# Optimization experiments

Hardware: AMD Instinct MI355X
Metric: run time of the kernel (lower is better)

The kernel has to match this reference:

```python
import jax, jax.numpy as jnp
import numpy as np

N_NODES = 100000
N_EDGES = 1600000
D = 64
NUM_GROUPS = 2


def setup_inputs() -> dict:
    key = jax.random.key(0)
    k_h, k_ws, k_wg, k_src, k_dst, k_grp = jax.random.split(key, 6)
    h = jax.random.normal(k_h, (N_NODES, D), dtype=jnp.float32)
    # nn.Linear(in, out, bias=False) weights have shape [out, in]
    W_self = jax.random.normal(k_ws, (D, D), dtype=jnp.float32) * (1.0 / np.sqrt(D))
    W_groups = jax.random.normal(k_wg, (NUM_GROUPS, D, D), dtype=jnp.float32) * (1.0 / np.sqrt(D))
    src = jax.random.randint(k_src, (N_EDGES,), 0, N_NODES, dtype=jnp.int32)
    dst = jax.random.randint(k_dst, (N_EDGES,), 0, N_NODES, dtype=jnp.int32)
    group_labels = jax.random.randint(k_grp, (N_NODES,), 0, NUM_GROUPS, dtype=jnp.int32)
    return {"h": h, "W_self": W_self, "W_groups": W_groups,
            "src": src, "dst": dst, "group_labels": group_labels}


def reference(h, W_self, W_groups, src, dst, group_labels):
    # h: [N, d_in]; W_self: [d_out, d_in]; W_groups: [G, d_out, d_in]
    # Edge list (src, dst) replaces the DGL graph; message m_e = h[src_e],
    # transformed by W_groups[group[src_e]], scatter-added into dst_e.
    n_nodes = h.shape[0]
    num_groups = W_groups.shape[0]

    h_self = h @ W_self.T                       # [N, d_out]

    h_src = jnp.take(h, src, axis=0)            # [E, d_in] edge gather
    g_src = jnp.take(group_labels, src, axis=0)  # [E]

    h_agg = jnp.zeros((n_nodes, W_groups.shape[1]), dtype=h.dtype)
    for i in range(num_groups):  # small fixed loop over groups
        masked = jnp.where((g_src == i)[:, None], h_src, 0.0)  # [E, d_in]
        # Linearity lets us aggregate first, then transform (same math as
        # transforming each message then scatter_add, but far less compute).
        seg = jax.ops.segment_sum(masked, dst, num_segments=n_nodes)  # [N, d_in]
        h_agg = h_agg + seg @ W_groups[i].T      # [N, d_out]

    return h_self + h_agg
```

## Files before the change

kernel.cpp:

```cpp
#include <hip/hip_runtime.h>

#define N_NODES 100000
#define N_EDGES 1600000
#define D 64
#define NB2 3125
#define NR 2
#define CAPB_R 384
#define LCAP 64
#define LSTR 68
#define SRC_MASK 0x1FFFF
#define NBB 782
#define ZOFF (N_NODES * 32)

typedef unsigned int u32;
typedef short bfrag8 __attribute__((ext_vector_type(8)));
typedef float f32x4 __attribute__((ext_vector_type(4)));


__device__ inline u32 pk_bf16(float lo, float hi) {
    u32 a = __float_as_uint(lo);
    a = (a + 0x7fffu + ((a >> 16) & 1u)) >> 16;
    u32 b = __float_as_uint(hi);
    b = (b + 0x7fffu + ((b >> 16) & 1u)) & 0xffff0000u;
    return a | b;
}

__global__ __launch_bounds__(256) void prep(const float* __restrict__ h,
                                            const float* __restrict__ W_self,
                                            const float* __restrict__ W_groups,
                                            const int* __restrict__ src,
                                            const int* __restrict__ dst,
                                            const int* __restrict__ grp,
                                            int* __restrict__ bcnt,
                                            int* __restrict__ buckets,
                                            u32* __restrict__ h_bf,
                                            u32* __restrict__ Wc) {
    __shared__ int hist[NB2];
    __shared__ int gbase[NB2];
    const int tid = threadIdx.x;
    const int bx = blockIdx.x;

    if (bx < NBB) {
        const int r = bx & (NR - 1);
        for (int b = tid; b < NB2; b += 256) hist[b] = 0;
        __syncthreads();

        int ent[8], bkt[8], rnk[8];
        const int e0 = bx * 2048;
#pragma unroll
        for (int i = 0; i < 8; ++i) {
            int e = e0 + tid + i * 256;
            if (e < N_EDGES) {
                int s = src[e], d = dst[e];
                int g = grp[s];
                bkt[i] = d >> 5;
                ent[i] = s | (g << 17) | ((d & 31) << 18);
                rnk[i] = atomicAdd(&hist[bkt[i]], 1);
            } else {
                bkt[i] = -1;
            }
        }
        __syncthreads();
        for (int b = tid; b < NB2; b += 256) {
            int hc = hist[b];
            gbase[b] = hc ? atomicAdd(&bcnt[b * NR + r], hc) : 0;
        }
        __syncthreads();
#pragma unroll
        for (int i = 0; i < 8; ++i) {
            if (bkt[i] >= 0) {
                int pos = gbase[bkt[i]] + rnk[i];
                if (pos < CAPB_R)
                    buckets[(bkt[i] * NR + r) * CAPB_R + pos] = ent[i];
            }
        }
    } else if (bx < NBB + 12500) {
        int i = (bx - NBB) * 256 + tid;
        float2 v = reinterpret_cast<const float2*>(h)[i];
        h_bf[i] = pk_bf16(v.x, v.y);
    } else {
        for (int idx = tid; idx < 6144; idx += 256) {
            int j = idx / 96, kk = idx - j * 96;
            int k = kk * 2;
            float lo, hi;
            if (k < 64)       { lo = W_self[j * 64 + k];          hi = W_self[j * 64 + k + 1]; }
            else if (k < 128) { lo = W_groups[j * 64 + k - 64];   hi = W_groups[j * 64 + k - 63]; }
            else              { lo = W_groups[4096 + j * 64 + k - 128];
                                hi = W_groups[4096 + j * 64 + k - 127]; }
            Wc[j * 96 + kk] = pk_bf16(lo, hi);
        }
        if (tid < 32) h_bf[ZOFF + tid] = 0u;
    }
}

__global__ __launch_bounds__(256, 8) void gather_gemm(const u32* __restrict__ h_bf,
                                                      const int* __restrict__ bcnt,
                                                      const int* __restrict__ buckets,
                                                      const u32* __restrict__ Wc,
                                                      float* __restrict__ out) {
    __shared__ __align__(16) int lcsr[32 * LSTR];
    __shared__ int cntg[64];

    const int tid = threadIdx.x;
    const int cb = blockIdx.x;
    const int nbase = cb * 32;

    if (tid < 64) cntg[tid] = 0;
    __syncthreads();

    {
        const int2 cc = *reinterpret_cast<const int2*>(bcnt + cb * NR);
        int cns[NR] = { cc.x, cc.y };
#pragma unroll
        for (int r = 0; r < NR; ++r) {
            const int cnt = min(cns[r], CAPB_R);
            const int* bp = buckets + (cb * NR + r) * CAPB_R;
            for (int i = tid; i < cnt; i += 256) {
                int e = bp[i];
                int nl = (e >> 18) & 31;
                int g = (e >> 17) & 1;
                int off = (e & SRC_MASK) * 32;
                int idx = atomicAdd(&cntg[g * 32 + nl], 1);
                int pos = g ? (LCAP - 1 - idx) : idx;
                if (idx < LCAP) lcsr[nl * LSTR + pos] = off;
            }
        }
    }
    __syncthreads();

    const int wave = tid >> 6;
    const int lane = tid & 63;
    const int half = lane >> 5;
    const int c = lane & 31;

    for (int q = 0; q < 8; ++q) {
        const int nl = wave * 8 + q;
        const int base = nl * LSTR;
        const int c0 = min(cntg[nl], LCAP);
        const int c1 = min(cntg[32 + nl], LCAP);
        const int total = c0 + c1;
        float a0l = 0.f, a0h = 0.f, a1l = 0.f, a1h = 0.f;

        for (int i = 0; i < total; i += 8) {
            if (i + 8 <= c0) {
                int off[4];
#pragma unroll
                for (int k = 0; k < 4; ++k)
                    off[k] = lcsr[base + i + 2 * k + half];
                u32 x[4];
#pragma unroll
                for (int k = 0; k < 4; ++k) x[k] = h_bf[(size_t)(off[k] + c)];
#pragma unroll
                for (int k = 0; k < 4; ++k) {
                    a0l += __uint_as_float(x[k] << 16);
                    a0h += __uint_as_float(x[k] & 0xffff0000u);
                }
            } else if (i >= c0) {
                int off[4];
#pragma unroll
                for (int k = 0; k < 4; ++k) {
                    int u = i + 2 * k + half;
                    int idx = (LCAP - 1 - (u - c0)) & (LCAP - 1);
                    int v = lcsr[base + idx];
                    off[k] = (u < total) ? v : ZOFF;
                }
                u32 x[4];
#pragma unroll
                for (int k = 0; k < 4; ++k) x[k] = h_bf[(size_t)(off[k] + c)];
#pragma unroll
                for (int k = 0; k < 4; ++k) {
                    a1l += __uint_as_float(x[k] << 16);
                    a1h += __uint_as_float(x[k] & 0xffff0000u);
                }
            } else {
                int off[4];
                bool fm[4];
#pragma unroll
                for (int k = 0; k < 4; ++k) {
                    int u = i + 2 * k + half;
                    bool f = u < c0;
                    int idx = f ? u : ((LCAP - 1 - (u - c0)) & (LCAP - 1));
                    int v = lcsr[base + idx];
                    off[k] = (u < total) ? v : ZOFF;
                    fm[k] = f;
                }
                u32 x[4];
#pragma unroll
                for (int k = 0; k < 4; ++k) x[k] = h_bf[(size_t)(off[k] + c)];
#pragma unroll
                for (int k = 0; k < 4; ++k) {
                    float vl = __uint_as_float(x[k] << 16);
                    float vh = __uint_as_float(x[k] & 0xffff0000u);
                    a0l += fm[k] ? vl : 0.f;
                    a0h += fm[k] ? vh : 0.f;
                    a1l += fm[k] ? 0.f : vl;
                    a1h += fm[k] ? 0.f : vh;
                }
            }
        }

        a0l += __shfl_xor(a0l, 32, 64);
        a0h += __shfl_xor(a0h, 32, 64);
        a1l += __shfl_xor(a1l, 32, 64);
        a1h += __shfl_xor(a1h, 32, 64);

        if (half == 0) {
            lcsr[base + c]      = (int)pk_bf16(a0l, a0h);
            lcsr[base + 32 + c] = (int)pk_bf16(a1l, a1h);
        }
    }
    __syncthreads();

    const int m = lane & 15;
    const int quad = lane >> 4;
    const int rowh = wave & 1;
    const int jth = wave >> 1;
    const int nl16 = rowh * 16 + m;
    const int arow = nbase + nl16;

    union Cvt { uint4 u; bfrag8 s; };
    bfrag8 a[6];
    const u32* ap = h_bf + (size_t)arow * 32 + quad * 4;
#pragma unroll
    for (int ks = 0; ks < 2; ++ks) {
        Cvt cv;
        cv.u = *reinterpret_cast<const uint4*>(ap + ks * 16);
        a[ks] = cv.s;
    }
#pragma unroll
    for (int ks = 2; ks < 6; ++ks) {
        Cvt cv;
        cv.u = *reinterpret_cast<const uint4*>(&lcsr[nl16 * LSTR + (ks - 2) * 16 + quad * 4]);
        a[ks] = cv.s;
    }

    f32x4 acc[2];
#pragma unroll
    for (int jj = 0; jj < 2; ++jj) acc[jj] = (f32x4){0.f, 0.f, 0.f, 0.f};

    const u32* wp = Wc + (size_t)m * 96 + quad * 4;
#pragma unroll
    for (int ks = 0; ks < 6; ++ks) {
#pragma unroll
        for (int jj = 0; jj < 2; ++jj) {
            Cvt cw;
            cw.u = *reinterpret_cast<const uint4*>(wp + (jth * 2 + jj) * 1536 + ks * 16);
            acc[jj] = __builtin_amdgcn_mfma_f32_16x16x32_bf16(a[ks], cw.s, acc[jj], 0, 0, 0);
        }
    }

    const int rbase = nbase + rowh * 16 + quad * 4;
#pragma unroll
    for (int jj = 0; jj < 2; ++jj) {
#pragma unroll
        for (int r = 0; r < 4; ++r) {
            out[(size_t)(rbase + r) * 64 + (jth * 2 + jj) * 16 + m] = acc[jj][r];
        }
    }
}

extern "C" void kernel_launch(void* const* d_in, const int* in_sizes, int n_in,
                              void* d_out, int out_size, void* d_ws, size_t ws_size,
                              hipStream_t stream) {
    const float* h        = (const float*)d_in[0];
    const float* W_self   = (const float*)d_in[1];
    const float* W_groups = (const float*)d_in[2];
    const int*   src      = (const int*)d_in[3];
    const int*   dst      = (const int*)d_in[4];
    const int*   grp      = (const int*)d_in[5];
    float*       out      = (float*)d_out;

    int* bcnt    = (int*)d_ws;
    int* buckets = bcnt + 8192;
    u32* h_bf    = (u32*)(buckets + NB2 * NR * CAPB_R);
    u32* Wc      = h_bf + (size_t)N_NODES * 32 + 32;

    hipMemsetAsync(bcnt, 0, 8192 * sizeof(int), stream);

    prep<<<NBB + 12500 + 1, 256, 0, stream>>>(h, W_self, W_groups, src, dst, grp,
                                              bcnt, buckets, h_bf, Wc);
    gather_gemm<<<NB2, 256, 0, stream>>>(h_bf, bcnt, buckets, Wc, out);
}
```

Measured before the change: 192.3 us.

## Use direct global atomics for bucketing and split the gather loop by group

The prep kernel drops its shared-memory histogram and two-pass bucket placement and instead takes one global atomicAdd per edge, choosing the sub-bucket from the edge index parity. Each packed entry now stores a byte offset so the gather can use it directly. The gather loop is split into separate per-group loops that read four offsets with one vector LDS load and skip the mixed-group masking. The bf16 conversion handles four floats per thread. The aim is fewer barriers and fewer instructions in the bucketing and gather stages, at the cost of much heavier global atomic contention on the bucket counters.

```diff
diff --git a/kernel.cpp b/kernel.cpp
--- a/kernel.cpp
+++ b/kernel.cpp
@@ -8,9 +8,9 @@
 #define CAPB_R 384
 #define LCAP 64
 #define LSTR 68
-#define SRC_MASK 0x1FFFF
 #define NBB 782
-#define ZOFF (N_NODES * 32)
+#define NTC 6250
+#define ZB ((u32)(N_NODES * 128))
 
 typedef unsigned int u32;
 typedef short bfrag8 __attribute__((ext_vector_type(8)));
@@ -35,17 +35,10 @@
                                             int* __restrict__ buckets,
                                             u32* __restrict__ h_bf,
                                             u32* __restrict__ Wc) {
-    __shared__ int hist[NB2];
-    __shared__ int gbase[NB2];
     const int tid = threadIdx.x;
     const int bx = blockIdx.x;
 
     if (bx < NBB) {
-        const int r = bx & (NR - 1);
-        for (int b = tid; b < NB2; b += 256) hist[b] = 0;
-        __syncthreads();
-
-        int ent[8], bkt[8], rnk[8];
         const int e0 = bx * 2048;
 #pragma unroll
         for (int i = 0; i < 8; ++i) {
@@ -53,31 +46,17 @@
             if (e < N_EDGES) {
                 int s = src[e], d = dst[e];
                 int g = grp[s];
-                bkt[i] = d >> 5;
-                ent[i] = s | (g << 17) | ((d & 31) << 18);
-                rnk[i] = atomicAdd(&hist[bkt[i]], 1);
-            } else {
-                bkt[i] = -1;
+                int cidx = (d >> 5) * NR + (e & 1);
+                u32 ent = ((u32)s << 7) | ((u32)g << 5) | (u32)(d & 31);
+                int pos = atomicAdd(&bcnt[cidx], 1);
+                if (pos < CAPB_R) buckets[cidx * CAPB_R + pos] = (int)ent;
             }
         }
-        __syncthreads();
-        for (int b = tid; b < NB2; b += 256) {
-            int hc = hist[b];
-            gbase[b] = hc ? atomicAdd(&bcnt[b * NR + r], hc) : 0;
-        }
-        __syncthreads();
-#pragma unroll
-        for (int i = 0; i < 8; ++i) {
-            if (bkt[i] >= 0) {
-                int pos = gbase[bkt[i]] + rnk[i];
-                if (pos < CAPB_R)
-                    buckets[(bkt[i] * NR + r) * CAPB_R + pos] = ent[i];
-            }
-        }
-    } else if (bx < NBB + 12500) {
+    } else if (bx < NBB + NTC) {
         int i = (bx - NBB) * 256 + tid;
-        float2 v = reinterpret_cast<const float2*>(h)[i];
-        h_bf[i] = pk_bf16(v.x, v.y);
+        float4 v = reinterpret_cast<const float4*>(h)[i];
+        h_bf[2 * i]     = pk_bf16(v.x, v.y);
+        h_bf[2 * i + 1] = pk_bf16(v.z, v.w);
     } else {
         for (int idx = tid; idx < 6144; idx += 256) {
             int j = idx / 96, kk = idx - j * 96;
@@ -89,7 +68,7 @@
                                 hi = W_groups[4096 + j * 64 + k - 127]; }
             Wc[j * 96 + kk] = pk_bf16(lo, hi);
         }
-        if (tid < 32) h_bf[ZOFF + tid] = 0u;
+        if (tid < 32) h_bf[N_NODES * 32 + tid] = 0u;
     }
 }
 
@@ -116,13 +95,13 @@
             const int cnt = min(cns[r], CAPB_R);
             const int* bp = buckets + (cb * NR + r) * CAPB_R;
             for (int i = tid; i < cnt; i += 256) {
-                int e = bp[i];
-                int nl = (e >> 18) & 31;
-                int g = (e >> 17) & 1;
-                int off = (e & SRC_MASK) * 32;
+                u32 e = (u32)bp[i];
+                int nl = e & 31;
+                int g = (e >> 5) & 1;
+                u32 off = e & 0xFFFFFF80u;
                 int idx = atomicAdd(&cntg[g * 32 + nl], 1);
                 int pos = g ? (LCAP - 1 - idx) : idx;
-                if (idx < LCAP) lcsr[nl * LSTR + pos] = off;
+                if (idx < LCAP) lcsr[nl * LSTR + pos] = (int)off;
             }
         }
     }
@@ -131,72 +110,72 @@
     const int wave = tid >> 6;
     const int lane = tid & 63;
     const int half = lane >> 5;
-    const int c = lane & 31;
+    const u32 c4 = (u32)((lane & 31) * 4);
+    const char* hb = (const char*)h_bf;
 
     for (int q = 0; q < 8; ++q) {
         const int nl = wave * 8 + q;
         const int base = nl * LSTR;
         const int c0 = min(cntg[nl], LCAP);
         const int c1 = min(cntg[32 + nl], LCAP);
-        const int total = c0 + c1;
         float a0l = 0.f, a0h = 0.f, a1l = 0.f, a1h = 0.f;
 
-        for (int i = 0; i < total; i += 8) {
-            if (i + 8 <= c0) {
-                int off[4];
-#pragma unroll
-                for (int k = 0; k < 4; ++k)
-                    off[k] = lcsr[base + i + 2 * k + half];
-                u32 x[4];
-#pragma unroll
-                for (int k = 0; k < 4; ++k) x[k] = h_bf[(size_t)(off[k] + c)];
-#pragma unroll
-                for (int k = 0; k < 4; ++k) {
-                    a0l += __uint_as_float(x[k] << 16);
-                    a0h += __uint_as_float(x[k] & 0xffff0000u);
-                }
-            } else if (i >= c0) {
-                int off[4];
-#pragma unroll
-                for (int k = 0; k < 4; ++k) {
-                    int u = i + 2 * k + half;
-                    int idx = (LCAP - 1 - (u - c0)) & (LCAP - 1);
-                    int v = lcsr[base + idx];
-                    off[k] = (u < total) ? v : ZOFF;
-                }
-                u32 x[4];
-#pragma unroll
-                for (int k = 0; k < 4; ++k) x[k] = h_bf[(size_t)(off[k] + c)];
-#pragma unroll
-                for (int k = 0; k < 4; ++k) {
-                    a1l += __uint_as_float(x[k] << 16);
-                    a1h += __uint_as_float(x[k] & 0xffff0000u);
-                }
-            } else {
-                int off[4];
-                bool fm[4];
-#pragma unroll
-                for (int k = 0; k < 4; ++k) {
-                    int u = i + 2 * k + half;
-                    bool f = u < c0;
-                    int idx = f ? u : ((LCAP - 1 - (u - c0)) & (LCAP - 1));
-                    int v = lcsr[base + idx];
-                    off[k] = (u < total) ? v : ZOFF;
-                    fm[k] = f;
-                }
-                u32 x[4];
-#pragma unroll
-                for (int k = 0; k < 4; ++k) x[k] = h_bf[(size_t)(off[k] + c)];
-#pragma unroll
-                for (int k = 0; k < 4; ++k) {
-                    float vl = __uint_as_float(x[k] << 16);
-                    float vh = __uint_as_float(x[k] & 0xffff0000u);
-                    a0l += fm[k] ? vl : 0.f;
-                    a0h += fm[k] ? vh : 0.f;
-                    a1l += fm[k] ? 0.f : vl;
-                    a1h += fm[k] ? 0.f : vh;
-                }
-            }
+        int i = 0;
+        for (; i + 8 <= c0; i += 8) {
+            int4 w = *reinterpret_cast<const int4*>(&lcsr[base + i + 4 * half]);
+            u32 x0 = *(const u32*)(hb + ((u32)w.x + c4));
+            u32 x1 = *(const u32*)(hb + ((u32)w.y + c4));
+            u32 x2 = *(const u32*)(hb + ((u32)w.z + c4));
+            u32 x3 = *(const u32*)(hb + ((u32)w.w + c4));
+            a0l += __uint_as_float(x0 << 16); a0h += __uint_as_float(x0 & 0xffff0000u);
+            a0l += __uint_as_float(x1 << 16); a0h += __uint_as_float(x1 & 0xffff0000u);
+            a0l += __uint_as_float(x2 << 16); a0h += __uint_as_float(x2 & 0xffff0000u);
+            a0l += __uint_as_float(x3 << 16); a0h += __uint_as_float(x3 & 0xffff0000u);
+        }
+        if (i < c0) {
+            int4 w = *reinterpret_cast<const int4*>(&lcsr[base + i + 4 * half]);
+            int u = i + 4 * half;
+            u32 o0 = (u + 0 < c0) ? (u32)w.x : ZB;
+            u32 o1 = (u + 1 < c0) ? (u32)w.y : ZB;
+            u32 o2 = (u + 2 < c0) ? (u32)w.z : ZB;
+            u32 o3 = (u + 3 < c0) ? (u32)w.w : ZB;
+            u32 x0 = *(const u32*)(hb + (o0 + c4));
+            u32 x1 = *(const u32*)(hb + (o1 + c4));
+            u32 x2 = *(const u32*)(hb + (o2 + c4));
+            u32 x3 = *(const u32*)(hb + (o3 + c4));
+            a0l += __uint_as_float(x0 << 16); a0h += __uint_as_float(x0 & 0xffff0000u);
+            a0l += __uint_as_float(x1 << 16); a0h += __uint_as_float(x1 & 0xffff0000u);
+            a0l += __uint_as_float(x2 << 16); a0h += __uint_as_float(x2 & 0xffff0000u);
+            a0l += __uint_as_float(x3 << 16); a0h += __uint_as_float(x3 & 0xffff0000u);
+        }
+
+        int j = 0;
+        for (; j + 8 <= c1; j += 8) {
+            int4 w = *reinterpret_cast<const int4*>(&lcsr[base + (LCAP - 4) - j - 4 * half]);
+            u32 x0 = *(const u32*)(hb + ((u32)w.x + c4));
+            u32 x1 = *(const u32*)(hb + ((u32)w.y + c4));
+            u32 x2 = *(const u32*)(hb + ((u32)w.z + c4));
+            u32 x3 = *(const u32*)(hb + ((u32)w.w + c4));
+            a1l += __uint_as_float(x0 << 16); a1h += __uint_as_float(x0 & 0xffff0000u);
+            a1l += __uint_as_float(x1 << 16); a1h += __uint_as_float(x1 & 0xffff0000u);
+            a1l += __uint_as_float(x2 << 16); a1h += __uint_as_float(x2 & 0xffff0000u);
+            a1l += __uint_as_float(x3 << 16); a1h += __uint_as_float(x3 & 0xffff0000u);
+        }
+        if (j < c1) {
+            int4 w = *reinterpret_cast<const int4*>(&lcsr[base + (LCAP - 4) - j - 4 * half]);
+            int u = j + 4 * half;
+            u32 o0 = (u + 3 < c1) ? (u32)w.x : ZB;
+            u32 o1 = (u + 2 < c1) ? (u32)w.y : ZB;
+            u32 o2 = (u + 1 < c1) ? (u32)w.z : ZB;
+            u32 o3 = (u + 0 < c1) ? (u32)w.w : ZB;
+            u32 x0 = *(const u32*)(hb + (o0 + c4));
+            u32 x1 = *(const u32*)(hb + (o1 + c4));
+            u32 x2 = *(const u32*)(hb + (o2 + c4));
+            u32 x3 = *(const u32*)(hb + (o3 + c4));
+            a1l += __uint_as_float(x0 << 16); a1h += __uint_as_float(x0 & 0xffff0000u);
+            a1l += __uint_as_float(x1 << 16); a1h += __uint_as_float(x1 & 0xffff0000u);
+            a1l += __uint_as_float(x2 << 16); a1h += __uint_as_float(x2 & 0xffff0000u);
+            a1l += __uint_as_float(x3 << 16); a1h += __uint_as_float(x3 & 0xffff0000u);
         }
 
         a0l += __shfl_xor(a0l, 32, 64);
@@ -205,6 +184,7 @@
         a1h += __shfl_xor(a1h, 32, 64);
 
         if (half == 0) {
+            const int c = lane & 31;
             lcsr[base + c]      = (int)pk_bf16(a0l, a0h);
             lcsr[base + 32 + c] = (int)pk_bf16(a1l, a1h);
         }
@@ -277,7 +257,7 @@
 
     hipMemsetAsync(bcnt, 0, 8192 * sizeof(int), stream);
 
-    prep<<<NBB + 12500 + 1, 256, 0, stream>>>(h, W_self, W_groups, src, dst, grp,
-                                              bcnt, buckets, h_bf, Wc);
+    prep<<<NBB + NTC + 1, 256, 0, stream>>>(h, W_self, W_groups, src, dst, grp,
+                                            bcnt, buckets, h_bf, Wc);
     gather_gemm<<<NB2, 256, 0, stream>>>(h_bf, bcnt, buckets, Wc, out);
 }
```

Result: slower. 224.6 us (+16.8%).
